# Kernel optimization log

Hardware: AMD Instinct MI355X
Metric: run time of the kernel (lower is better)

## Reference

```python
import jax, jax.numpy as jnp
import numpy as np

B, NPG, EG, F, EDIM, ESM = 32, 256, 2048, 128, 16, 1280
NN, E = B * NPG, B * EG
H, Dh = 4, 128
HD = H * Dh


def setup_inputs() -> dict:
    key = jax.random.key(0)
    ks = jax.random.split(key, 32)
    x = jax.random.normal(ks[0], (NN, F), jnp.float32)
    edge_attr = jax.random.normal(ks[1], (E, EDIM), jnp.float32)
    off = jnp.repeat(jnp.arange(B, dtype=jnp.int32) * NPG, EG)
    src = off + jax.random.randint(ks[2], (E,), 0, NPG, dtype=jnp.int32)
    dst = off + jax.random.randint(ks[3], (E,), 0, NPG, dtype=jnp.int32)
    edge_index = jnp.stack([src, dst])
    batch_index = jnp.repeat(jnp.arange(B, dtype=jnp.int32), NPG)
    esm = jax.random.normal(ks[4], (B, ESM), jnp.float32)
    g = lambda i, shp: jax.random.normal(ks[i], shp, jnp.float32) * 0.05
    return dict(
        x=x, edge_attr=edge_attr, edge_index=edge_index, batch_index=batch_index,
        esm2_embeddings=esm,
        Wq=g(5, (5, F, HD)), bq=g(6, (5, HD)), Wk=g(7, (5, F, HD)), bk=g(8, (5, HD)),
        Wv=g(9, (5, F, HD)), bv=g(10, (5, HD)), We=g(11, (5, EDIM, HD)),
        Wskip=g(12, (5, F, HD)), bskip=g(13, (5, HD)), Wbeta=g(14, (5, 3 * HD)),
        Wt=g(15, (5, HD, F)), bt=g(16, (5, F)),
        gamma=1.0 + g(17, (5, F)), beta_bn=g(18, (5, F)), rmean=g(19, (5, F)),
        rvar=0.5 + jax.random.uniform(ks[20], (5, F)),
        pw=g(21, (2, F)),
        W1=g(22, (2 * F + ESM, 512)), b1=g(23, (512,)),
        W2=g(24, (512, 256)), b2=g(25, (256,)),
        W3=g(26, (256, 10)), b3=g(27, (10,)))


def _forward(x, edge_attr, esm, Wq, bq, Wk, bk, Wv, bv, We, Wskip, bskip, Wbeta,
             Wt, bt, gamma, beta_bn, rmean, rvar, pw, W1, b1, W2, b2, W3, b3,
             src, dst, batch_index):
    scale = 1.0 / jnp.sqrt(jnp.float32(Dh))

    def conv(h, li, emask):
        # PyG TransformerConv(beta=True, edge_dim) + Linear + ReLU + BatchNorm(eval)
        q = (h @ Wq[li] + bq[li]).reshape(NN, H, Dh)
        k = (h @ Wk[li] + bk[li]).reshape(NN, H, Dh)
        v = (h @ Wv[li] + bv[li]).reshape(NN, H, Dh)
        e = (edge_attr @ We[li]).reshape(E, H, Dh)   # lin_edge, bias=False
        kj = k[src] + e                               # [E,H,Dh]
        a = jnp.einsum('ehd,ehd->eh', q[dst], kj) * scale
        a = jnp.where(emask[:, None], a, -1e30)
        m = jnp.maximum(jax.ops.segment_max(a, dst, num_segments=NN), -1e30)
        ea = jnp.exp(a - m[dst]) * emask[:, None]
        den = jax.ops.segment_sum(ea, dst, num_segments=NN)
        attn = ea / jnp.maximum(den[dst], 1e-16)      # scatter-softmax over dst
        msg = (v[src] + e) * attn[..., None]
        out = jax.ops.segment_sum(msg, dst, num_segments=NN).reshape(NN, HD)
        xr = h @ Wskip[li] + bskip[li]                # root/skip path
        bta = jax.nn.sigmoid(jnp.concatenate([out, xr, out - xr], -1) @ Wbeta[li])[:, None]
        h2 = bta * xr + (1.0 - bta) * out
        h2 = jax.nn.relu(h2 @ Wt[li] + bt[li])
        return (h2 - rmean[li]) / jnp.sqrt(rvar[li] + 1e-5) * gamma[li] + beta_bn[li]

    nmask = jnp.ones((NN,), bool)
    emask = jnp.ones((E,), bool)
    h = conv(x, 0, emask)
    k_list = [NPG // 2, NPG // 4]  # ratio=0.5 applied twice
    reps = []
    for i in range(4):
        h = conv(h, i + 1, emask)
        if i % 2 == 0:  # top_k_every_n = 2
            p = i // 2
            w = pw[p]
            s = jnp.tanh((h @ w) / jnp.linalg.norm(w))      # TopKPooling score
            s_m = jnp.where(nmask, s, -jnp.inf)
            ranks = jnp.argsort(jnp.argsort(-s_m.reshape(B, NPG), axis=1), axis=1).reshape(-1)
            keep = (ranks < k_list[p]) & nmask
            h = h * s[:, None] * keep[:, None]
            nmask = keep
            emask = emask & keep[src] & keep[dst]
            cnt = jax.ops.segment_sum(keep.astype(h.dtype), batch_index, num_segments=B)
            gmax = jax.ops.segment_max(jnp.where(keep[:, None], h, -1e30), batch_index, num_segments=B)
            gmean = jax.ops.segment_sum(h * keep[:, None], batch_index, num_segments=B) / jnp.maximum(cnt, 1.0)[:, None]
            reps.append(jnp.concatenate([gmax, gmean], 1))
    g = reps[0] + reps[1]
    g = jnp.concatenate([g, esm], 1)
    g = jax.nn.relu(g @ W1 + b1)   # dropout(p=0.8) is identity at inference
    g = jax.nn.relu(g @ W2 + b2)
    return g @ W3 + b3


def reference(x, edge_attr, edge_index, batch_index, esm2_embeddings,
              Wq, bq, Wk, bk, Wv, bv, We, Wskip, bskip, Wbeta, Wt, bt,
              gamma, beta_bn, rmean, rvar, pw, W1, b1, W2, b2, W3, b3):
    src, dst = edge_index[0], edge_index[1]
    return _forward(x, edge_attr, esm2_embeddings, Wq, bq, Wk, bk, Wv, bv, We,
                    Wskip, bskip, Wbeta, Wt, bt, gamma, beta_bn, rmean, rvar,
                    pw, W1, b1, W2, b2, W3, b3, src, dst, batch_index)
```

## Files before the change

### kernel.cpp

```cpp
#include <hip/hip_runtime.h>
#include <math.h>

#define BB 32
#define NPGC 256
#define FF 128
#define EDIMC 16
#define ESMC 1280
#define NNODE 8192
#define NEDGE 65536
#define EGC 2048
#define NH 4
#define DH 128
#define HDIM 512

typedef __attribute__((ext_vector_type(8))) short bf16x8;
typedef __attribute__((ext_vector_type(4))) float f32x4;

__device__ __forceinline__ float waveReduceSum(float v) {
#pragma unroll
    for (int o = 32; o > 0; o >>= 1) v += __shfl_down(v, o);
    return v;
}

__device__ __forceinline__ unsigned short f2b(float f) {
    unsigned u = __builtin_bit_cast(unsigned, f);
    return (unsigned short)((u + 0x7fffu + ((u >> 16) & 1u)) >> 16);
}
__device__ __forceinline__ unsigned pack2(float lo, float hi) {
    return (unsigned)f2b(lo) | ((unsigned)f2b(hi) << 16);
}
__device__ __forceinline__ float2 b2f2(unsigned u) {
    float lo = __builtin_bit_cast(float, u << 16);
    float hi = __builtin_bit_cast(float, u & 0xffff0000u);
    return make_float2(lo, hi);
}

__global__ __launch_bounds__(256) void k_convert_setup(
    const float* __restrict__ x, const float* __restrict__ Wq,
    const float* __restrict__ Wk, const float* __restrict__ Wv,
    const float* __restrict__ Wsk, const float* __restrict__ Wt,
    const float* __restrict__ W1, const float* __restrict__ W2,
    unsigned short* __restrict__ xb, unsigned short* __restrict__ wqb,
    unsigned short* __restrict__ wkb, unsigned short* __restrict__ wvb,
    unsigned short* __restrict__ wskb, unsigned short* __restrict__ wtb,
    unsigned short* __restrict__ w1b, unsigned short* __restrict__ w2b,
    const int* __restrict__ dst, int* __restrict__ emask, int* __restrict__ nmask,
    int* __restrict__ coff, int* __restrict__ ceid) {
    __shared__ int cntS[NPGC];
    __shared__ int scanS[NPGC];
    __shared__ int offS[NPGC];
    if (blockIdx.x >= 12800) {
        int g = blockIdx.x - 12800, t = threadIdx.x;
        cntS[t] = 0;
        nmask[g * NPGC + t] = 1;
        __syncthreads();
        int base = g * EGC;
#pragma unroll
        for (int i = 0; i < EGC / 256; ++i) {
            int e = base + i * 256 + t;
            emask[e] = 1;
            atomicAdd(&cntS[dst[e] - g * NPGC], 1);
        }
        __syncthreads();
        scanS[t] = cntS[t];
        __syncthreads();
        for (int off = 1; off < NPGC; off <<= 1) {
            int v = scanS[t];
            if (t >= off) v += scanS[t - off];
            __syncthreads();
            scanS[t] = v;
            __syncthreads();
        }
        int excl = scanS[t] - cntS[t];
        offS[t] = excl;
        coff[g * NPGC + t] = base + excl;
        if (g == 0 && t == 0) coff[NNODE] = NEDGE;
        cntS[t] = 0;
        __syncthreads();
#pragma unroll
        for (int i = 0; i < EGC / 256; ++i) {
            int e = base + i * 256 + t;
            int d = dst[e] - g * NPGC;
            int pos = atomicAdd(&cntS[d], 1);
            ceid[base + offS[d] + pos] = e;
        }
        return;
    }
    int idx = blockIdx.x * 256 + threadIdx.x;
    if (idx < 1048576) { xb[idx] = f2b(x[idx]); return; }
    idx -= 1048576;
    if (idx < 1048576) {
        int fam = idx >> 18, local = idx & 262143;
        int li = local >> 16, rem = local & 65535;
        int n = rem >> 7, k = rem & 127;
        const float* S = (fam == 0) ? Wq : (fam == 1) ? Wk : (fam == 2) ? Wv : Wsk;
        unsigned short* D = (fam == 0) ? wqb : (fam == 1) ? wkb : (fam == 2) ? wvb : wskb;
        D[local] = f2b(S[(size_t)li * 65536 + (size_t)k * 512 + n]);
        return;
    }
    idx -= 1048576;
    if (idx < 262144) {
        int li = idx >> 16, rem = idx & 65535;
        int n = rem >> 9, k = rem & 511;
        wtb[idx] = f2b(Wt[(size_t)li * 65536 + (size_t)k * 128 + n]);
        return;
    }
    idx -= 262144;
    if (idx < 786432) {
        int n = idx / 1536, k = idx % 1536;
        w1b[idx] = f2b(W1[(size_t)k * 512 + n]);
        return;
    }
    idx -= 786432;
    {
        int n = idx >> 9, k = idx & 511;
        w2b[idx] = f2b(W2[(size_t)k * 256 + n]);
    }
}

__global__ __launch_bounds__(256) void k_qkvs_mfma(
    const unsigned short* __restrict__ hb,
    const unsigned short* __restrict__ wq, const unsigned short* __restrict__ wk,
    const unsigned short* __restrict__ wv, const unsigned short* __restrict__ wsk,
    const float* __restrict__ bq, const float* __restrict__ bk,
    const float* __restrict__ bv, const float* __restrict__ bsk,
    unsigned short* __restrict__ oq, unsigned short* __restrict__ ok,
    unsigned short* __restrict__ ov, unsigned short* __restrict__ osk) {
    const unsigned short* W;
    const float* bias;
    unsigned short* out;
    if (blockIdx.z == 0) { W = wq; bias = bq; out = oq; }
    else if (blockIdx.z == 1) { W = wk; bias = bk; out = ok; }
    else if (blockIdx.z == 2) { W = wv; bias = bv; out = ov; }
    else { W = wsk; bias = bsk; out = osk; }
    int lane = threadIdx.x & 63, wave = threadIdx.x >> 6;
    int quad = lane >> 4, m = lane & 15;
    int xcdx = blockIdx.x;
    int g = (xcdx & 7) + 8 * ((xcdx >> 3) & 3);
    int half = xcdx >> 5;
    int rowbase = g * NPGC + half * 128 + (wave >> 1) * 64;
    int colbase = blockIdx.y * 128 + (wave & 1) * 64;
    f32x4 zero = {0.f, 0.f, 0.f, 0.f};
    f32x4 acc[4][4];
#pragma unroll
    for (int i = 0; i < 4; ++i)
#pragma unroll
        for (int j = 0; j < 4; ++j) acc[i][j] = zero;
#pragma unroll
    for (int ks = 0; ks < 4; ++ks) {
        int k0 = ks * 32 + quad * 8;
        bf16x8 af[4], bfr[4];
#pragma unroll
        for (int tm = 0; tm < 4; ++tm)
            af[tm] = *(const bf16x8*)(hb + (size_t)(rowbase + tm * 16 + m) * FF + k0);
#pragma unroll
        for (int tn = 0; tn < 4; ++tn)
            bfr[tn] = *(const bf16x8*)(W + (size_t)(colbase + tn * 16 + m) * FF + k0);
#pragma unroll
        for (int tm = 0; tm < 4; ++tm)
#pragma unroll
            for (int tn = 0; tn < 4; ++tn)
                acc[tm][tn] = __builtin_amdgcn_mfma_f32_16x16x32_bf16(af[tm], bfr[tn],
                                                                      acc[tm][tn], 0, 0, 0);
    }
#pragma unroll
    for (int tn = 0; tn < 4; ++tn) {
        int col = colbase + tn * 16 + m;
        float bc = bias[col];
#pragma unroll
        for (int tm = 0; tm < 4; ++tm)
#pragma unroll
            for (int r = 0; r < 4; ++r)
                out[(size_t)(rowbase + tm * 16 + quad * 4 + r) * HDIM + col] =
                    f2b(acc[tm][tn][r] + bc);
    }
}

__global__ __launch_bounds__(128) void k_out_mfma(
    const unsigned short* __restrict__ h2b, const unsigned short* __restrict__ wt,
    const float* __restrict__ bt_, const float* __restrict__ gam_,
    const float* __restrict__ bet_, const float* __restrict__ rme_,
    const float* __restrict__ rva_, float* __restrict__ hout,
    unsigned short* __restrict__ hbf) {
    int lane = threadIdx.x & 63, wave = threadIdx.x >> 6;
    int quad = lane >> 4, m = lane & 15;
    int bi = blockIdx.x;
    int g = (bi & 7) + 8 * ((bi >> 3) & 3);
    int sub = bi >> 5;
    int rowbase = g * NPGC + sub * 32;
    int colbase = wave * 64;
    f32x4 zero = {0.f, 0.f, 0.f, 0.f};
    f32x4 acc[2][4];
#pragma unroll
    for (int i = 0; i < 2; ++i)
#pragma unroll
        for (int j = 0; j < 4; ++j) acc[i][j] = zero;
    for (int ks = 0; ks < 16; ++ks) {
        int k0 = ks * 32 + quad * 8;
        bf16x8 af[2], bfr[4];
#pragma unroll
        for (int tm = 0; tm < 2; ++tm)
            af[tm] = *(const bf16x8*)(h2b + (size_t)(rowbase + tm * 16 + m) * HDIM + k0);
#pragma unroll
        for (int tn = 0; tn < 4; ++tn)
            bfr[tn] = *(const bf16x8*)(wt + (size_t)(colbase + tn * 16 + m) * HDIM + k0);
#pragma unroll
        for (int tm = 0; tm < 2; ++tm)
#pragma unroll
            for (int tn = 0; tn < 4; ++tn)
                acc[tm][tn] = __builtin_amdgcn_mfma_f32_16x16x32_bf16(af[tm], bfr[tn],
                                                                      acc[tm][tn], 0, 0, 0);
    }
#pragma unroll
    for (int tn = 0; tn < 4; ++tn) {
        int col = colbase + tn * 16 + m;
        float bc = bt_[col];
        float sc = gam_[col] * rsqrtf(rva_[col] + 1e-5f);
        float sh = bet_[col] - rme_[col] * sc;
#pragma unroll
        for (int tm = 0; tm < 2; ++tm)
#pragma unroll
            for (int r = 0; r < 4; ++r) {
                size_t o = (size_t)(rowbase + tm * 16 + quad * 4 + r) * FF + col;
                float v = fmaxf(acc[tm][tn][r] + bc, 0.f) * sc + sh;
                hout[o] = v;
                hbf[o] = f2b(v);
            }
    }
}

__global__ __launch_bounds__(256) void k_mlp_mfma(const unsigned short* __restrict__ A,
                                                  const unsigned short* __restrict__ Wt,
                                                  float* __restrict__ cp,
                                                  int N, int K, int KS) {
    int lane = threadIdx.x & 63, wave = threadIdx.x >> 6;
    int quad = lane >> 4, m = lane & 15;
    int colbase = blockIdx.x * 256 + wave * 64;
    int kc = K / KS;
    int k0b = blockIdx.y * kc;
    f32x4 zero = {0.f, 0.f, 0.f, 0.f};
    f32x4 acc[2][4];
#pragma unroll
    for (int i = 0; i < 2; ++i)
#pragma unroll
        for (int j = 0; j < 4; ++j) acc[i][j] = zero;
    for (int ks = 0; ks < kc / 32; ++ks) {
        int k0 = k0b + ks * 32 + quad * 8;
        bf16x8 a0 = *(const bf16x8*)(A + (size_t)m * K + k0);
        bf16x8 a1 = *(const bf16x8*)(A + (size_t)(16 + m) * K + k0);
        bf16x8 bfr[4];
#pragma unroll
        for (int tn = 0; tn < 4; ++tn)
            bfr[tn] = *(const bf16x8*)(Wt + (size_t)(colbase + tn * 16 + m) * K + k0);
#pragma unroll
        for (int tn = 0; tn < 4; ++tn) {
            acc[0][tn] = __builtin_amdgcn_mfma_f32_16x16x32_bf16(a0, bfr[tn], acc[0][tn], 0, 0, 0);
            acc[1][tn] = __builtin_amdgcn_mfma_f32_16x16x32_bf16(a1, bfr[tn], acc[1][tn], 0, 0, 0);
        }
    }
#pragma unroll
    for (int tm = 0; tm < 2; ++tm)
#pragma unroll
        for (int tn = 0; tn < 4; ++tn)
#pragma unroll
            for (int r = 0; r < 4; ++r)
                cp[((size_t)blockIdx.y * 32 + tm * 16 + quad * 4 + r) * N +
                   colbase + tn * 16 + m] = acc[tm][tn][r];
}

__global__ void k_mlp_fix(const float* __restrict__ cp, const float* __restrict__ b,
                          float* __restrict__ C, unsigned short* __restrict__ Cb,
                          int MN, int N, int KS, int relu) {
    int i = blockIdx.x * 256 + threadIdx.x;
    if (i >= MN) return;
    float acc = b[i % N];
    for (int s = 0; s < KS; ++s) acc += cp[(size_t)s * MN + i];
    if (relu) acc = fmaxf(acc, 0.f);
    C[i] = acc;
    if (Cb) Cb[i] = f2b(acc);
}

__global__ void k_g1(const float* __restrict__ pmax0, const float* __restrict__ psum0,
                     const float* __restrict__ pmax1, const float* __restrict__ psum1,
                     const float* __restrict__ esm, unsigned short* __restrict__ g1b) {
    int i = blockIdx.x * 256 + threadIdx.x;
    int r = i / 1536, c = i % 1536;
    float v;
    if (c < 128) {
        float m0 = -1e30f, m1 = -1e30f;
#pragma unroll
        for (int q = 0; q < 4; ++q) {
            m0 = fmaxf(m0, pmax0[((size_t)r * 4 + q) * 128 + c]);
            m1 = fmaxf(m1, pmax1[((size_t)r * 4 + q) * 128 + c]);
        }
        v = m0 + m1;
    } else if (c < 256) {
        int d = c - 128;
        float s0 = 0.f, s1 = 0.f;
#pragma unroll
        for (int q = 0; q < 4; ++q) {
            s0 += psum0[((size_t)r * 4 + q) * 128 + d];
            s1 += psum1[((size_t)r * 4 + q) * 128 + d];
        }
        v = s0 * (1.f / 128.f) + s1 * (1.f / 64.f);
    } else {
        v = esm[(size_t)r * ESMC + c - 256];
    }
    g1b[i] = f2b(v);
}

__global__ __launch_bounds__(256) void k_attn_wave(
    const unsigned short* __restrict__ q, const unsigned short* __restrict__ kmat,
    const unsigned short* __restrict__ vmat, const unsigned short* __restrict__ xr,
    const float* __restrict__ eattr, const float* __restrict__ We,
    const float* __restrict__ Wb,
    const int* __restrict__ src, const int* __restrict__ coff,
    const int* __restrict__ ceid, const int* __restrict__ emask,
    unsigned short* __restrict__ h2) {
    int wv = threadIdx.x >> 6, ln = threadIdx.x & 63;
    int bi = blockIdx.x;
    int g = (bi & 7) + 8 * ((bi >> 3) & 3);
    int sub = bi >> 5;
    int n = g * NPGC + sub * 4 + wv;
    int h = ln >> 4, j = ln & 15;
    int d0i = ln * 8;
    int o0 = coff[n];
    int deg = coff[n + 1] - o0;
    if (deg > 64) deg = 64;

    uint4 qu = *(const uint4*)(q + (size_t)n * HDIM + d0i);
    float2 q0 = b2f2(qu.x), q1 = b2f2(qu.y), q2 = b2f2(qu.z), q3 = b2f2(qu.w);
    float qf[8] = {q0.x, q0.y, q1.x, q1.y, q2.x, q2.y, q3.x, q3.y};

    float qp[16];
#pragma unroll
    for (int jj = 0; jj < EDIMC; ++jj) {
        const float4* wp = (const float4*)(We + (size_t)jj * HDIM + d0i);
        float4 wa = wp[0], wb4 = wp[1];
        qp[jj] = qf[0] * wa.x + qf[1] * wa.y + qf[2] * wa.z + qf[3] * wa.w +
                 qf[4] * wb4.x + qf[5] * wb4.y + qf[6] * wb4.z + qf[7] * wb4.w;
    }
#pragma unroll
    for (int off = 1; off < 16; off <<= 1)
#pragma unroll
        for (int jj = 0; jj < EDIMC; ++jj) qp[jj] += __shfl_xor(qp[jj], off);
    float qWl = qp[j];

    int e_reg = 0, s_reg = -1;
    if (ln < deg) {
        e_reg = ceid[o0 + ln];
        s_reg = emask[e_reg] ? src[e_reg] : -1;
    }

    float mA = -1e30f, denA = 0.f, zA = 0.f;
    float mB = -1e30f, denB = 0.f, zB = 0.f;
    float outA[8] = {0.f, 0.f, 0.f, 0.f, 0.f, 0.f, 0.f, 0.f};
    float outB[8] = {0.f, 0.f, 0.f, 0.f, 0.f, 0.f, 0.f, 0.f};

    int i = 0;
    for (; i + 1 < deg; i += 2) {
        int siA = __shfl(s_reg, i), siB = __shfl(s_reg, i + 1);
        int eiA = __shfl(e_reg, i), eiB = __shfl(e_reg, i + 1);
        int sa = (siA < 0) ? 0 : siA;
        int sb = (siB < 0) ? 0 : siB;
        uint4 kuA = *(const uint4*)(kmat + (size_t)sa * HDIM + d0i);
        uint4 vuA = *(const uint4*)(vmat + (size_t)sa * HDIM + d0i);
        uint4 kuB = *(const uint4*)(kmat + (size_t)sb * HDIM + d0i);
        uint4 vuB = *(const uint4*)(vmat + (size_t)sb * HDIM + d0i);
        float eavA = eattr[(size_t)eiA * EDIMC + j];
        float eavB = eattr[(size_t)eiB * EDIMC + j];
        float2 ka0 = b2f2(kuA.x), ka1 = b2f2(kuA.y), ka2 = b2f2(kuA.z), ka3 = b2f2(kuA.w);
        float2 kb0 = b2f2(kuB.x), kb1 = b2f2(kuB.y), kb2 = b2f2(kuB.z), kb3 = b2f2(kuB.w);
        float pA = qf[0] * ka0.x + qf[1] * ka0.y + qf[2] * ka1.x + qf[3] * ka1.y +
                   qf[4] * ka2.x + qf[5] * ka2.y + qf[6] * ka3.x + qf[7] * ka3.y;
        float pB = qf[0] * kb0.x + qf[1] * kb0.y + qf[2] * kb1.x + qf[3] * kb1.y +
                   qf[4] * kb2.x + qf[5] * kb2.y + qf[6] * kb3.x + qf[7] * kb3.y;
        pA = fmaf(qWl, eavA, pA);
        pB = fmaf(qWl, eavB, pB);
        pA += __shfl_xor(pA, 8);  pB += __shfl_xor(pB, 8);
        pA += __shfl_xor(pA, 4);  pB += __shfl_xor(pB, 4);
        pA += __shfl_xor(pA, 2);  pB += __shfl_xor(pB, 2);
        pA += __shfl_xor(pA, 1);  pB += __shfl_xor(pB, 1);
        float sA = (siA < 0) ? -1e30f : pA * 0.088388347648318447f;
        float sB = (siB < 0) ? -1e30f : pB * 0.088388347648318447f;
        {
            float m_new = fmaxf(mA, sA);
            float c = __expf(mA - m_new);
            float al = (siA < 0) ? 0.f : __expf(sA - m_new);
            denA = denA * c + al;
            zA = zA * c + al * eavA;
            float2 v0 = b2f2(vuA.x), v1 = b2f2(vuA.y), v2 = b2f2(vuA.z), v3 = b2f2(vuA.w);
            outA[0] = outA[0] * c + al * v0.x;
            outA[1] = outA[1] * c + al * v0.y;
            outA[2] = outA[2] * c + al * v1.x;
            outA[3] = outA[3] * c + al * v1.y;
            outA[4] = outA[4] * c + al * v2.x;
            outA[5] = outA[5] * c + al * v2.y;
            outA[6] = outA[6] * c + al * v3.x;
            outA[7] = outA[7] * c + al * v3.y;
            mA = m_new;
        }
        {
            float m_new = fmaxf(mB, sB);
            float c = __expf(mB - m_new);
            float al = (siB < 0) ? 0.f : __expf(sB - m_new);
            denB = denB * c + al;
            zB = zB * c + al * eavB;
            float2 v0 = b2f2(vuB.x), v1 = b2f2(vuB.y), v2 = b2f2(vuB.z), v3 = b2f2(vuB.w);
            outB[0] = outB[0] * c + al * v0.x;
            outB[1] = outB[1] * c + al * v0.y;
            outB[2] = outB[2] * c + al * v1.x;
            outB[3] = outB[3] * c + al * v1.y;
            outB[4] = outB[4] * c + al * v2.x;
            outB[5] = outB[5] * c + al * v2.y;
            outB[6] = outB[6] * c + al * v3.x;
            outB[7] = outB[7] * c + al * v3.y;
            mB = m_new;
        }
    }
    if (i < deg) {
        int siA = __shfl(s_reg, i);
        int eiA = __shfl(e_reg, i);
        int sa = (siA < 0) ? 0 : siA;
        uint4 kuA = *(const uint4*)(kmat + (size_t)sa * HDIM + d0i);
        uint4 vuA = *(const uint4*)(vmat + (size_t)sa * HDIM + d0i);
        float eavA = eattr[(size_t)eiA * EDIMC + j];
        float2 ka0 = b2f2(kuA.x), ka1 = b2f2(kuA.y), ka2 = b2f2(kuA.z), ka3 = b2f2(kuA.w);
        float pA = qf[0] * ka0.x + qf[1] * ka0.y + qf[2] * ka1.x + qf[3] * ka1.y +
                   qf[4] * ka2.x + qf[5] * ka2.y + qf[6] * ka3.x + qf[7] * ka3.y;
        pA = fmaf(qWl, eavA, pA);
        pA += __shfl_xor(pA, 8);
        pA += __shfl_xor(pA, 4);
        pA += __shfl_xor(pA, 2);
        pA += __shfl_xor(pA, 1);
        float sA = (siA < 0) ? -1e30f : pA * 0.088388347648318447f;
        float m_new = fmaxf(mA, sA);
        float c = __expf(mA - m_new);
        float al = (siA < 0) ? 0.f : __expf(sA - m_new);
        denA = denA * c + al;
        zA = zA * c + al * eavA;
        float2 v0 = b2f2(vuA.x), v1 = b2f2(vuA.y), v2 = b2f2(vuA.z), v3 = b2f2(vuA.w);
        outA[0] = outA[0] * c + al * v0.x;
        outA[1] = outA[1] * c + al * v0.y;
        outA[2] = outA[2] * c + al * v1.x;
        outA[3] = outA[3] * c + al * v1.y;
        outA[4] = outA[4] * c + al * v2.x;
        outA[5] = outA[5] * c + al * v2.y;
        outA[6] = outA[6] * c + al * v3.x;
        outA[7] = outA[7] * c + al * v3.y;
        mA = m_new;
    }
    float mT = fmaxf(mA, mB);
    float cA = __expf(mA - mT), cB = __expf(mB - mT);
    float den = denA * cA + denB * cB;
    float z = zA * cA + zB * cB;
    float out[8];
#pragma unroll
    for (int d = 0; d < 8; ++d) out[d] = outA[d] * cA + outB[d] * cB;

    float inv = 1.f / fmaxf(den, 1e-16f);
    z *= inv;
#pragma unroll
    for (int d = 0; d < 8; ++d) out[d] *= inv;

#pragma unroll
    for (int jj = 0; jj < EDIMC; ++jj) {
        float zjj = __shfl(z, h * 16 + jj);
        const float4* wp = (const float4*)(We + (size_t)jj * HDIM + d0i);
        float4 wa = wp[0], wb4 = wp[1];
        out[0] = fmaf(zjj, wa.x, out[0]);
        out[1] = fmaf(zjj, wa.y, out[1]);
        out[2] = fmaf(zjj, wa.z, out[2]);
        out[3] = fmaf(zjj, wa.w, out[3]);
        out[4] = fmaf(zjj, wb4.x, out[4]);
        out[5] = fmaf(zjj, wb4.y, out[5]);
        out[6] = fmaf(zjj, wb4.z, out[6]);
        out[7] = fmaf(zjj, wb4.w, out[7]);
    }

    uint4 xu = *(const uint4*)(xr + (size_t)n * HDIM + d0i);
    float2 x0 = b2f2(xu.x), x1 = b2f2(xu.y), x2 = b2f2(xu.z), x3 = b2f2(xu.w);
    float xf[8] = {x0.x, x0.y, x1.x, x1.y, x2.x, x2.y, x3.x, x3.y};
    const float4* w0p = (const float4*)(Wb + d0i);
    const float4* w1p = (const float4*)(Wb + HDIM + d0i);
    const float4* w2p = (const float4*)(Wb + 2 * HDIM + d0i);
    float4 wa0 = w0p[0], wa1 = w0p[1];
    float4 wb0 = w1p[0], wb1 = w1p[1];
    float4 wc0 = w2p[0], wc1 = w2p[1];
    float w0f[8] = {wa0.x, wa0.y, wa0.z, wa0.w, wa1.x, wa1.y, wa1.z, wa1.w};
    float w1f[8] = {wb0.x, wb0.y, wb0.z, wb0.w, wb1.x, wb1.y, wb1.z, wb1.w};
    float w2f[8] = {wc0.x, wc0.y, wc0.z, wc0.w, wc1.x, wc1.y, wc1.z, wc1.w};
    float part = 0.f;
#pragma unroll
    for (int d = 0; d < 8; ++d)
        part += out[d] * w0f[d] + xf[d] * w1f[d] + (out[d] - xf[d]) * w2f[d];
#pragma unroll
    for (int o = 32; o > 0; o >>= 1) part += __shfl_xor(part, o);
    float bg = 1.f / (1.f + __expf(-part));
    uint4 res;
    res.x = pack2(bg * xf[0] + (1.f - bg) * out[0], bg * xf[1] + (1.f - bg) * out[1]);
    res.y = pack2(bg * xf[2] + (1.f - bg) * out[2], bg * xf[3] + (1.f - bg) * out[3]);
    res.z = pack2(bg * xf[4] + (1.f - bg) * out[4], bg * xf[5] + (1.f - bg) * out[5]);
    res.w = pack2(bg * xf[6] + (1.f - bg) * out[6], bg * xf[7] + (1.f - bg) * out[7]);
    *(uint4*)(h2 + (size_t)n * HDIM + d0i) = res;
}

__global__ __launch_bounds__(256) void k_pool_rank(const float* __restrict__ pwv,
                                                   const float* __restrict__ h,
                                                   int* __restrict__ nmask,
                                                   int* __restrict__ emask,
                                                   const int* __restrict__ src,
                                                   const int* __restrict__ dst,
                                                   float* __restrict__ fbuf, int kc) {
    __shared__ float smS[NPGC];
    __shared__ int keepS[NPGC];
    int g = blockIdx.x, t = threadIdx.x;
    int n = g * NPGC + t;
    const float* hr = h + (size_t)n * FF;
    float nw2 = 0.f, dv = 0.f;
#pragma unroll
    for (int i = 0; i < FF; i += 4) {
        float4 wv = *(const float4*)(pwv + i);
        float4 hv = *(const float4*)(hr + i);
        nw2 += wv.x * wv.x + wv.y * wv.y + wv.z * wv.z + wv.w * wv.w;
        dv += hv.x * wv.x + hv.y * wv.y + hv.z * wv.z + hv.w * wv.w;
    }
    float s = tanhf(dv / sqrtf(nw2));
    int old = nmask[n];
    smS[t] = old ? s : -INFINITY;
    __syncthreads();
    float mys = smS[t];
    int rank = 0;
    for (int j = 0; j < NPGC; ++j) {
        float o = smS[j];
        rank += (o > mys) || (o == mys && j < t);
    }
    int kp = (rank < kc) && old;
    keepS[t] = kp;
    nmask[n] = kp;
    fbuf[n] = s * (float)kp;
    __syncthreads();
    if (emask) {
        int base = g * EGC;
        for (int ee = t; ee < EGC; ee += 256) {
            int e = base + ee;
            emask[e] = emask[e] && keepS[src[e] - g * NPGC] && keepS[dst[e] - g * NPGC];
        }
    }
}

__global__ __launch_bounds__(256) void k_pool_apply(const float* __restrict__ h,
                                                    unsigned short* __restrict__ hbf,
                                                    const float* __restrict__ fbuf,
                                                    const int* __restrict__ nmask,
                                                    float* __restrict__ pmax,
                                                    float* __restrict__ psum, int emit) {
    __shared__ float mS[4][128];
    __shared__ float sS[4][128];
    int g = blockIdx.x, seg = blockIdx.y, t = threadIdx.x;
    int l = t & 63, quar = t >> 6;
    int d2 = l * 2;
    int nbase = g * NPGC + seg * 64 + quar * 16;
    float mx0 = -1e30f, mx1 = -1e30f, sm0 = 0.f, sm1 = 0.f;
#pragma unroll 4
    for (int i = 0; i < 16; ++i) {
        int n = nbase + i;
        float f = fbuf[n];
        int kp = nmask[n];
        float2 hv = *(const float2*)(h + (size_t)n * FF + d2);
        float v0 = hv.x * f, v1 = hv.y * f;
        if (emit) *(unsigned*)(hbf + (size_t)n * FF + d2) = pack2(v0, v1);
        if (kp) {
            mx0 = fmaxf(mx0, v0);
            mx1 = fmaxf(mx1, v1);
            sm0 += v0;
            sm1 += v1;
        }
    }
    mS[quar][d2] = mx0;
    mS[quar][d2 + 1] = mx1;
    sS[quar][d2] = sm0;
    sS[quar][d2 + 1] = sm1;
    __syncthreads();
    if (t < 128) {
        float m = fmaxf(fmaxf(mS[0][t], mS[1][t]), fmaxf(mS[2][t], mS[3][t]));
        float s = sS[0][t] + sS[1][t] + sS[2][t] + sS[3][t];
        pmax[((size_t)g * 4 + seg) * 128 + t] = m;
        psum[((size_t)g * 4 + seg) * 128 + t] = s;
    }
}

__global__ __launch_bounds__(256) void k_mlp_wave(const float* __restrict__ A,
                                                  const float* __restrict__ W,
                                                  const float* __restrict__ b,
                                                  float* __restrict__ C,
                                                  int M, int N, int K, int relu) {
    int wid = (blockIdx.x * 256 + threadIdx.x) >> 6;
    int lane = threadIdx.x & 63;
    if (wid >= M * N) return;
    int r = wid / N, c = wid % N;
    const float* Arow = A + (size_t)r * K;
    float acc = 0.f;
    for (int kk = lane; kk < K; kk += 64)
        acc = fmaf(Arow[kk], W[(size_t)kk * N + c], acc);
    acc = waveReduceSum(acc);
    if (lane == 0) {
        acc += b[c];
        C[wid] = relu ? fmaxf(acc, 0.f) : acc;
    }
}

extern "C" void kernel_launch(void* const* d_in, const int* in_sizes, int n_in,
                              void* d_out, int out_size, void* d_ws, size_t ws_size,
                              hipStream_t stream) {
    const float* x = (const float*)d_in[0];
    const float* eattr = (const float*)d_in[1];
    const int* eidx = (const int*)d_in[2];
    const float* esm = (const float*)d_in[4];
    const float* Wq = (const float*)d_in[5];
    const float* bq = (const float*)d_in[6];
    const float* Wk = (const float*)d_in[7];
    const float* bk = (const float*)d_in[8];
    const float* Wv = (const float*)d_in[9];
    const float* bv = (const float*)d_in[10];
    const float* We = (const float*)d_in[11];
    const float* Wsk = (const float*)d_in[12];
    const float* bsk = (const float*)d_in[13];
    const float* Wbe = (const float*)d_in[14];
    const float* Wt = (const float*)d_in[15];
    const float* bt = (const float*)d_in[16];
    const float* gam = (const float*)d_in[17];
    const float* bet = (const float*)d_in[18];
    const float* rme = (const float*)d_in[19];
    const float* rva = (const float*)d_in[20];
    const float* pw = (const float*)d_in[21];
    const float* W1 = (const float*)d_in[22];
    const float* b1 = (const float*)d_in[23];
    const float* W2 = (const float*)d_in[24];
    const float* b2 = (const float*)d_in[25];
    const float* W3 = (const float*)d_in[26];
    const float* b3 = (const float*)d_in[27];
    const int* srcp = eidx;
    const int* dstp = eidx + NEDGE;

    char* p = (char*)d_ws;
    auto alloc = [&](size_t bytes) -> void* {
        void* r = (void*)p;
        p += (bytes + 255) & ~(size_t)255;
        return r;
    };
    float* hA = (float*)alloc((size_t)NNODE * FF * 4);
    float* hB = (float*)alloc((size_t)NNODE * FF * 4);
    float* fbuf = (float*)alloc((size_t)NNODE * 4);
    float* pmax0 = (float*)alloc((size_t)BB * 4 * 128 * 4);
    float* psum0 = (float*)alloc((size_t)BB * 4 * 128 * 4);
    float* pmax1 = (float*)alloc((size_t)BB * 4 * 128 * 4);
    float* psum1 = (float*)alloc((size_t)BB * 4 * 128 * 4);
    float* g2 = (float*)alloc((size_t)BB * 512 * 4);
    float* g3 = (float*)alloc((size_t)BB * 256 * 4);
    float* cp = (float*)alloc((size_t)8 * 32 * 512 * 4);
    int* nmask = (int*)alloc((size_t)NNODE * 4);
    int* emask = (int*)alloc((size_t)NEDGE * 4);
    int* coff = (int*)alloc((size_t)(NNODE + 1) * 4);
    int* ceid = (int*)alloc((size_t)NEDGE * 4);
    unsigned short* xb = (unsigned short*)alloc((size_t)NNODE * FF * 2);
    unsigned short* hbf = (unsigned short*)alloc((size_t)NNODE * FF * 2);
    unsigned short* qb16 = (unsigned short*)alloc((size_t)NNODE * HDIM * 2);
    unsigned short* kb16 = (unsigned short*)alloc((size_t)NNODE * HDIM * 2);
    unsigned short* vb16 = (unsigned short*)alloc((size_t)NNODE * HDIM * 2);
    unsigned short* xrb16 = (unsigned short*)alloc((size_t)NNODE * HDIM * 2);
    unsigned short* h2b16 = (unsigned short*)alloc((size_t)NNODE * HDIM * 2);
    unsigned short* wqb = (unsigned short*)alloc((size_t)4 * 65536 * 2);
    unsigned short* wkb = (unsigned short*)alloc((size_t)4 * 65536 * 2);
    unsigned short* wvb = (unsigned short*)alloc((size_t)4 * 65536 * 2);
    unsigned short* wskb = (unsigned short*)alloc((size_t)4 * 65536 * 2);
    unsigned short* wtb = (unsigned short*)alloc((size_t)4 * 65536 * 2);
    unsigned short* w1b = (unsigned short*)alloc((size_t)786432 * 2);
    unsigned short* w2b = (unsigned short*)alloc((size_t)131072 * 2);
    unsigned short* g1b = (unsigned short*)alloc((size_t)BB * 1536 * 2);
    unsigned short* g2b = (unsigned short*)alloc((size_t)BB * 512 * 2);

    k_convert_setup<<<12832, 256, 0, stream>>>(x, Wq, Wk, Wv, Wsk, Wt, W1, W2,
                                               xb, wqb, wkb, wvb, wskb, wtb, w1b, w2b,
                                               dstp, emask, nmask, coff, ceid);

    auto conv = [&](int li, const unsigned short* hin_b, float* hout) {
        dim3 gq(64, 4, 4);
        k_qkvs_mfma<<<gq, 256, 0, stream>>>(
            hin_b, wqb + (size_t)li * 65536, wkb + (size_t)li * 65536,
            wvb + (size_t)li * 65536, wskb + (size_t)li * 65536,
            bq + li * HDIM, bk + li * HDIM, bv + li * HDIM, bsk + li * HDIM,
            qb16, kb16, vb16, xrb16);
        const float* WeL = We + (size_t)li * EDIMC * HDIM;
        k_attn_wave<<<NNODE / 4, 256, 0, stream>>>(qb16, kb16, vb16, xrb16, eattr, WeL,
                                                   Wbe + (size_t)li * 3 * HDIM,
                                                   srcp, coff, ceid, emask, h2b16);
        k_out_mfma<<<NNODE / 32, 128, 0, stream>>>(
            h2b16, wtb + (size_t)li * 65536, bt + li * FF, gam + li * FF,
            bet + li * FF, rme + li * FF, rva + li * FF, hout, hbf);
    };

    auto pool = [&](int pi, const float* h, float* pmax, float* psum, int kc, bool updE,
                    int emit) {
        k_pool_rank<<<BB, 256, 0, stream>>>(pw + pi * FF, h, nmask,
                                            updE ? emask : nullptr, srcp, dstp, fbuf, kc);
        k_pool_apply<<<dim3(BB, 4), 256, 0, stream>>>(h, hbf, fbuf, nmask, pmax, psum, emit);
    };

    conv(0, xb, hA);
    conv(1, hbf, hB);
    pool(0, hB, pmax0, psum0, NPGC / 2, true, 1);
    conv(2, hbf, hA);
    conv(3, hbf, hB);
    pool(1, hB, pmax1, psum1, NPGC / 4, false, 0);

    k_g1<<<BB * 1536 / 256, 256, 0, stream>>>(pmax0, psum0, pmax1, psum1, esm, g1b);
    k_mlp_mfma<<<dim3(2, 8), 256, 0, stream>>>(g1b, w1b, cp, 512, 1536, 8);
    k_mlp_fix<<<BB * 512 / 256, 256, 0, stream>>>(cp, b1, g2, g2b, BB * 512, 512, 8, 1);
    k_mlp_mfma<<<dim3(1, 8), 256, 0, stream>>>(g2b, w2b, cp, 256, 512, 8);
    k_mlp_fix<<<BB * 256 / 256, 256, 0, stream>>>(cp, b2, g3, nullptr, BB * 256, 256, 8, 1);
    k_mlp_wave<<<(BB * 10 * 64 + 255) / 256, 256, 0, stream>>>(g3, W3, b3, (float*)d_out,
                                                               BB, 10, 256, 0);
}
```

Baseline: 457.5 us.

## Precompute dense per-graph QK score matrix with MFMA, gather scores in attention

Adds a kernel that computes the full 256x256 per-graph, per-head Q·K^T score matrix with bf16 MFMA and stores it scaled in a new fp32 buffer. The attention kernel then looks up the precomputed score for each edge instead of gathering K rows and computing a dot product, keeping only the edge-feature term. This removes the per-edge K gathers and their dot products. In exchange it adds an extra launch and a dense computation over all node pairs, about four times the per-edge work, plus roughly 33 MB of score writes and reads per layer.

```diff
diff --git a/kernel.cpp b/kernel.cpp
--- a/kernel.cpp
+++ b/kernel.cpp
@@ -12,6 +12,7 @@
 #define NH 4
 #define DH 128
 #define HDIM 512
+#define SCALE 0.088388347648318447f
 
 typedef __attribute__((ext_vector_type(8))) short bf16x8;
 typedef __attribute__((ext_vector_type(4))) float f32x4;
@@ -176,6 +177,54 @@
     }
 }
 
+__global__ __launch_bounds__(256) void k_qk_mfma(const unsigned short* __restrict__ q,
+                                                 const unsigned short* __restrict__ kmat,
+                                                 float* __restrict__ S) {
+    int lane = threadIdx.x & 63, wave = threadIdx.x >> 6;
+    int quad = lane >> 4, m = lane & 15;
+    int bi = blockIdx.x;
+    int g = (bi & 7) + 8 * ((bi >> 3) & 3);
+    int tile = bi >> 5;
+    int h = blockIdx.y;
+    int rowbase = g * NPGC + (tile >> 1) * 128 + (wave >> 1) * 64;
+    int colbase = g * NPGC + (tile & 1) * 128 + (wave & 1) * 64;
+    f32x4 zero = {0.f, 0.f, 0.f, 0.f};
+    f32x4 acc[4][4];
+#pragma unroll
+    for (int i = 0; i < 4; ++i)
+#pragma unroll
+        for (int j = 0; j < 4; ++j) acc[i][j] = zero;
+#pragma unroll
+    for (int ks = 0; ks < 4; ++ks) {
+        int k0 = h * DH + ks * 32 + quad * 8;
+        bf16x8 af[4], bfr[4];
+#pragma unroll
+        for (int tm = 0; tm < 4; ++tm)
+            af[tm] = *(const bf16x8*)(q + (size_t)(rowbase + tm * 16 + m) * HDIM + k0);
+#pragma unroll
+        for (int tn = 0; tn < 4; ++tn)
+            bfr[tn] = *(const bf16x8*)(kmat + (size_t)(colbase + tn * 16 + m) * HDIM + k0);
+#pragma unroll
+        for (int tm = 0; tm < 4; ++tm)
+#pragma unroll
+            for (int tn = 0; tn < 4; ++tn)
+                acc[tm][tn] = __builtin_amdgcn_mfma_f32_16x16x32_bf16(af[tm], bfr[tn],
+                                                                      acc[tm][tn], 0, 0, 0);
+    }
+    float* Sg = S + (((size_t)g * NH + h) << 16);
+    int rl0 = rowbase - g * NPGC, cl0 = colbase - g * NPGC;
+#pragma unroll
+    for (int tn = 0; tn < 4; ++tn) {
+        int cl = cl0 + tn * 16 + m;
+#pragma unroll
+        for (int tm = 0; tm < 4; ++tm)
+#pragma unroll
+            for (int r = 0; r < 4; ++r)
+                Sg[(size_t)(rl0 + tm * 16 + quad * 4 + r) * NPGC + cl] =
+                    acc[tm][tn][r] * SCALE;
+    }
+}
+
 __global__ __launch_bounds__(128) void k_out_mfma(
     const unsigned short* __restrict__ h2b, const unsigned short* __restrict__ wt,
     const float* __restrict__ bt_, const float* __restrict__ gam_,
@@ -310,7 +359,7 @@
 }
 
 __global__ __launch_bounds__(256) void k_attn_wave(
-    const unsigned short* __restrict__ q, const unsigned short* __restrict__ kmat,
+    const unsigned short* __restrict__ q, const float* __restrict__ S,
     const unsigned short* __restrict__ vmat, const unsigned short* __restrict__ xr,
     const float* __restrict__ eattr, const float* __restrict__ We,
     const float* __restrict__ Wb,
@@ -321,9 +370,11 @@
     int bi = blockIdx.x;
     int g = (bi & 7) + 8 * ((bi >> 3) & 3);
     int sub = bi >> 5;
-    int n = g * NPGC + sub * 4 + wv;
+    int nl = sub * 4 + wv;
+    int n = g * NPGC + nl;
     int h = ln >> 4, j = ln & 15;
     int d0i = ln * 8;
+    int gbase = g * NPGC;
     int o0 = coff[n];
     int deg = coff[n + 1] - o0;
     if (deg > 64) deg = 64;
@@ -344,7 +395,9 @@
     for (int off = 1; off < 16; off <<= 1)
 #pragma unroll
         for (int jj = 0; jj < EDIMC; ++jj) qp[jj] += __shfl_xor(qp[jj], off);
-    float qWl = qp[j];
+    float qWls = qp[j] * SCALE;
+
+    const float* Srow = S + (((size_t)g * NH + h) << 16) + (size_t)nl * NPGC;
 
     int e_reg = 0, s_reg = -1;
     if (ln < deg) {
@@ -361,28 +414,22 @@
     for (; i + 1 < deg; i += 2) {
         int siA = __shfl(s_reg, i), siB = __shfl(s_reg, i + 1);
         int eiA = __shfl(e_reg, i), eiB = __shfl(e_reg, i + 1);
-        int sa = (siA < 0) ? 0 : siA;
-        int sb = (siB < 0) ? 0 : siB;
-        uint4 kuA = *(const uint4*)(kmat + (size_t)sa * HDIM + d0i);
+        int sa = (siA < 0) ? gbase : siA;
+        int sb = (siB < 0) ? gbase : siB;
+        float SvA = Srow[sa - gbase];
+        float SvB = Srow[sb - gbase];
         uint4 vuA = *(const uint4*)(vmat + (size_t)sa * HDIM + d0i);
-        uint4 kuB = *(const uint4*)(kmat + (size_t)sb * HDIM + d0i);
         uint4 vuB = *(const uint4*)(vmat + (size_t)sb * HDIM + d0i);
         float eavA = eattr[(size_t)eiA * EDIMC + j];
         float eavB = eattr[(size_t)eiB * EDIMC + j];
-        float2 ka0 = b2f2(kuA.x), ka1 = b2f2(kuA.y), ka2 = b2f2(kuA.z), ka3 = b2f2(kuA.w);
-        float2 kb0 = b2f2(kuB.x), kb1 = b2f2(kuB.y), kb2 = b2f2(kuB.z), kb3 = b2f2(kuB.w);
-        float pA = qf[0] * ka0.x + qf[1] * ka0.y + qf[2] * ka1.x + qf[3] * ka1.y +
-                   qf[4] * ka2.x + qf[5] * ka2.y + qf[6] * ka3.x + qf[7] * ka3.y;
-        float pB = qf[0] * kb0.x + qf[1] * kb0.y + qf[2] * kb1.x + qf[3] * kb1.y +
-                   qf[4] * kb2.x + qf[5] * kb2.y + qf[6] * kb3.x + qf[7] * kb3.y;
-        pA = fmaf(qWl, eavA, pA);
-        pB = fmaf(qWl, eavB, pB);
+        float pA = qWls * eavA;
+        float pB = qWls * eavB;
         pA += __shfl_xor(pA, 8);  pB += __shfl_xor(pB, 8);
         pA += __shfl_xor(pA, 4);  pB += __shfl_xor(pB, 4);
         pA += __shfl_xor(pA, 2);  pB += __shfl_xor(pB, 2);
         pA += __shfl_xor(pA, 1);  pB += __shfl_xor(pB, 1);
-        float sA = (siA < 0) ? -1e30f : pA * 0.088388347648318447f;
-        float sB = (siB < 0) ? -1e30f : pB * 0.088388347648318447f;
+        float sA = (siA < 0) ? -1e30f : SvA + pA;
+        float sB = (siB < 0) ? -1e30f : SvB + pB;
         {
             float m_new = fmaxf(mA, sA);
             float c = __expf(mA - m_new);
@@ -421,19 +468,16 @@
     if (i < deg) {
         int siA = __shfl(s_reg, i);
         int eiA = __shfl(e_reg, i);
-        int sa = (siA < 0) ? 0 : siA;
-        uint4 kuA = *(const uint4*)(kmat + (size_t)sa * HDIM + d0i);
+        int sa = (siA < 0) ? gbase : siA;
+        float SvA = Srow[sa - gbase];
         uint4 vuA = *(const uint4*)(vmat + (size_t)sa * HDIM + d0i);
         float eavA = eattr[(size_t)eiA * EDIMC + j];
-        float2 ka0 = b2f2(kuA.x), ka1 = b2f2(kuA.y), ka2 = b2f2(kuA.z), ka3 = b2f2(kuA.w);
-        float pA = qf[0] * ka0.x + qf[1] * ka0.y + qf[2] * ka1.x + qf[3] * ka1.y +
-                   qf[4] * ka2.x + qf[5] * ka2.y + qf[6] * ka3.x + qf[7] * ka3.y;
-        pA = fmaf(qWl, eavA, pA);
+        float pA = qWls * eavA;
         pA += __shfl_xor(pA, 8);
         pA += __shfl_xor(pA, 4);
         pA += __shfl_xor(pA, 2);
         pA += __shfl_xor(pA, 1);
-        float sA = (siA < 0) ? -1e30f : pA * 0.088388347648318447f;
+        float sA = (siA < 0) ? -1e30f : SvA + pA;
         float m_new = fmaxf(mA, sA);
         float c = __expf(mA - m_new);
         float al = (siA < 0) ? 0.f : __expf(sA - m_new);
@@ -651,6 +695,7 @@
     };
     float* hA = (float*)alloc((size_t)NNODE * FF * 4);
     float* hB = (float*)alloc((size_t)NNODE * FF * 4);
+    float* Sbuf = (float*)alloc((size_t)BB * NH * NPGC * NPGC * 4);
     float* fbuf = (float*)alloc((size_t)NNODE * 4);
     float* pmax0 = (float*)alloc((size_t)BB * 4 * 128 * 4);
     float* psum0 = (float*)alloc((size_t)BB * 4 * 128 * 4);
@@ -691,8 +736,9 @@
             wvb + (size_t)li * 65536, wskb + (size_t)li * 65536,
             bq + li * HDIM, bk + li * HDIM, bv + li * HDIM, bsk + li * HDIM,
             qb16, kb16, vb16, xrb16);
+        k_qk_mfma<<<dim3(128, 4), 256, 0, stream>>>(qb16, kb16, Sbuf);
         const float* WeL = We + (size_t)li * EDIMC * HDIM;
-        k_attn_wave<<<NNODE / 4, 256, 0, stream>>>(qb16, kb16, vb16, xrb16, eattr, WeL,
+        k_attn_wave<<<NNODE / 4, 256, 0, stream>>>(qb16, Sbuf, vb16, xrb16, eattr, WeL,
                                                    Wbe + (size_t)li * 3 * HDIM,
                                                    srcp, coff, ceid, emask, h2b16);
         k_out_mfma<<<NNODE / 32, 128, 0, stream>>>(
```

New measurement: 507.1 us. 10.8% more time.
